# Performance work log

Measured on AMD Instinct MI355X. Metric: run time of the kernel, lower is better.

## Reference

```python
import jax, jax.numpy as jnp
import numpy as np

N, E, D_IN, D_HID, D_OUT = 50000, 800000, 128, 128, 300
BN_EPS = 1e-5


def setup_inputs() -> dict:
    key = jax.random.key(0)
    ks = jax.random.split(key, 10)
    s_in = 1.0 / np.sqrt(D_IN)
    s_hid = 1.0 / np.sqrt(D_HID)
    return {
        "x": jax.random.normal(ks[0], (N, D_IN), jnp.float32),
        "edge_index": jax.random.randint(ks[1], (2, E), 0, N, jnp.int64),
        "Wl": jax.random.normal(ks[2], (D_IN, D_HID), jnp.float32) * s_in,
        "bl": jnp.zeros((D_HID,), jnp.float32),
        "Wr": jax.random.normal(ks[3], (D_IN, D_HID), jnp.float32) * s_in,
        "Wsk": jax.random.normal(ks[4], (D_IN, D_HID), jnp.float32) * s_in,
        "bsk": jnp.zeros((D_HID,), jnp.float32),
        "gamma": jnp.ones((D_HID,), jnp.float32),
        "beta": jnp.zeros((D_HID,), jnp.float32),
        "rmean": jnp.zeros((D_HID,), jnp.float32),
        "rvar": jnp.ones((D_HID,), jnp.float32),
        "Wlo": jax.random.normal(ks[5], (D_HID, D_OUT), jnp.float32) * s_hid,
        "blo": jnp.zeros((D_OUT,), jnp.float32),
        "Wro": jax.random.normal(ks[6], (D_HID, D_OUT), jnp.float32) * s_hid,
    }


def sage_conv(x, src, dst, n_nodes, W_l, b_l, W_r):
    # PyG SAGEConv (aggr='mean'): lin_l(mean_{j in N(i)} x_j) + lin_r(x_i)
    msgs = x[src]                                                 # [E, d] gather
    agg = jax.ops.segment_sum(msgs, dst, num_segments=n_nodes)    # [N, d]
    cnt = jax.ops.segment_sum(jnp.ones((src.shape[0], 1), x.dtype), dst,
                              num_segments=n_nodes)               # [N, 1]
    mean = agg / jnp.maximum(cnt, 1.0)
    return mean @ W_l + b_l + x @ W_r


def reference(x, edge_index, Wl, bl, Wr, Wsk, bsk, gamma, beta, rmean, rvar,
              Wlo, blo, Wro):
    src, dst = edge_index[0], edge_index[1]
    n = x.shape[0]
    # layer 0: conv + skip linear
    h = sage_conv(x, src, dst, n, Wl, bl, Wr) + (x @ Wsk + bsk)
    # BatchNorm1d (eval: running stats)
    h = (h - rmean) * (gamma * jax.lax.rsqrt(rvar + BN_EPS)) + beta
    x_emb = jax.nn.relu(h)                                        # dropout: no-op in eval
    # output conv + log_softmax
    x_out = sage_conv(x_emb, src, dst, n, Wlo, blo, Wro)
    return h, jax.nn.log_softmax(x_out, axis=1)
```

## Files before the change

### kernel.cpp

```cpp
#include <hip/hip_runtime.h>

typedef __attribute__((__ext_vector_type__(8))) __bf16 bf16x8;
typedef __attribute__((__ext_vector_type__(4))) float f32x4;
typedef __attribute__((__ext_vector_type__(2))) float f32x2;
typedef __attribute__((__ext_vector_type__(4))) unsigned int u32x4;

__device__ __forceinline__ float bf2f(unsigned short u) {
    return __uint_as_float(((unsigned int)u) << 16);
}
__device__ __forceinline__ unsigned short f2bf(float f) {
    unsigned int u = __float_as_uint(f);
    u += 0x7FFFu + ((u >> 16) & 1u);
    return (unsigned short)(u >> 16);
}

__device__ __forceinline__ bool low_short_is_bf16like(unsigned int w) {
    unsigned int lo = w & 0xFFFFu;
    if (lo == 0u || lo == 0x8000u) return true;
    unsigned int e = (lo >> 7) & 0xFFu;
    return (e >= 0x6Cu && e <= 0x8Cu);
}
__device__ __forceinline__ int probe_f32(const unsigned int* __restrict__ p) {
    int t = threadIdx.x & 63;
    int cnt = __popcll(__ballot(low_short_is_bf16like(p[t])));
    return (cnt < 32) ? 1 : 0;
}
__device__ __forceinline__ int probe_e64(const unsigned int* __restrict__ ei) {
    int t = threadIdx.x & 63;
    unsigned int o1 = ei[2 * t + 1];
    unsigned int o2 = ei[2 * t + 129];
    return __all((o1 == 0u) && (o2 == 0u)) ? 1 : 0;
}

__global__ __launch_bounds__(256) void k_tobf(
    const void* __restrict__ xv, unsigned short* __restrict__ xbf,
    unsigned int* __restrict__ x8, int* __restrict__ deg,
    long nelem, int n, int tgrid)
{
    if ((int)blockIdx.x >= tgrid) {
        int j = ((int)blockIdx.x - tgrid) * 256 + threadIdx.x;
        if (j < n) deg[j] = 0;
        return;
    }
    int xf32 = probe_f32((const unsigned int*)xv);
    long i = ((long)blockIdx.x * 256 + threadIdx.x) * 8;
    if (i >= nelem) return;
    float f[8];
    if (xf32) {
        const float4* p = (const float4*)((const float*)xv + i);
        float4 v0 = p[0], v1 = p[1];
        f[0] = v0.x; f[1] = v0.y; f[2] = v0.z; f[3] = v0.w;
        f[4] = v1.x; f[5] = v1.y; f[6] = v1.z; f[7] = v1.w;
        u32x4 o;
        o.x = (unsigned int)f2bf(f[0]) | ((unsigned int)f2bf(f[1]) << 16);
        o.y = (unsigned int)f2bf(f[2]) | ((unsigned int)f2bf(f[3]) << 16);
        o.z = (unsigned int)f2bf(f[4]) | ((unsigned int)f2bf(f[5]) << 16);
        o.w = (unsigned int)f2bf(f[6]) | ((unsigned int)f2bf(f[7]) << 16);
        *(u32x4*)&xbf[i] = o;
    } else {
        u32x4 v = *(const u32x4*)((const unsigned short*)xv + i);
        *(u32x4*)&xbf[i] = v;
        f[0] = bf2f((unsigned short)v.x); f[1] = bf2f((unsigned short)(v.x >> 16));
        f[2] = bf2f((unsigned short)v.y); f[3] = bf2f((unsigned short)(v.y >> 16));
        f[4] = bf2f((unsigned short)v.z); f[5] = bf2f((unsigned short)(v.z >> 16));
        f[6] = bf2f((unsigned short)v.w); f[7] = bf2f((unsigned short)(v.w >> 16));
    }
    unsigned int q0 = 0, q1 = 0;
    q0 = (unsigned int)__builtin_amdgcn_cvt_pk_fp8_f32(f[0], f[1], (int)q0, false);
    q0 = (unsigned int)__builtin_amdgcn_cvt_pk_fp8_f32(f[2], f[3], (int)q0, true);
    q1 = (unsigned int)__builtin_amdgcn_cvt_pk_fp8_f32(f[4], f[5], (int)q1, false);
    q1 = (unsigned int)__builtin_amdgcn_cvt_pk_fp8_f32(f[6], f[7], (int)q1, true);
    uint2 q; q.x = q0; q.y = q1;
    *(uint2*)&x8[i >> 2] = q;
}

__global__ __launch_bounds__(256) void k_to8(
    const unsigned short* __restrict__ src, unsigned int* __restrict__ dst,
    long nelem)
{
    long i = ((long)blockIdx.x * 256 + threadIdx.x) * 8;
    if (i >= nelem) return;
    u32x4 v = *(const u32x4*)&src[i];
    unsigned int q0 = 0, q1 = 0;
    q0 = (unsigned int)__builtin_amdgcn_cvt_pk_fp8_f32(
            bf2f((unsigned short)v.x), bf2f((unsigned short)(v.x >> 16)), (int)q0, false);
    q0 = (unsigned int)__builtin_amdgcn_cvt_pk_fp8_f32(
            bf2f((unsigned short)v.y), bf2f((unsigned short)(v.y >> 16)), (int)q0, true);
    q1 = (unsigned int)__builtin_amdgcn_cvt_pk_fp8_f32(
            bf2f((unsigned short)v.z), bf2f((unsigned short)(v.z >> 16)), (int)q1, false);
    q1 = (unsigned int)__builtin_amdgcn_cvt_pk_fp8_f32(
            bf2f((unsigned short)v.w), bf2f((unsigned short)(v.w >> 16)), (int)q1, true);
    uint2 q; q.x = q0; q.y = q1;
    *(uint2*)&dst[i >> 2] = q;
}

__global__ __launch_bounds__(256) void k_fold(
    const void* __restrict__ Wl, const void* __restrict__ Wr,
    const void* __restrict__ Wsk, const void* __restrict__ gamma,
    const void* __restrict__ rvar, const void* __restrict__ bl,
    const void* __restrict__ bsk, const void* __restrict__ rmean,
    const void* __restrict__ beta, const void* __restrict__ Wlo,
    const void* __restrict__ blo, const void* __restrict__ Wro,
    unsigned short* __restrict__ W1p, unsigned short* __restrict__ W2p,
    float* __restrict__ bias1, float* __restrict__ bias2)
{
    int wf32 = probe_f32((const unsigned int*)Wl);
    int b = blockIdx.x, t = threadIdx.x;
    if (b < 128) {
        int idx = b * 256 + t;
        int kb = idx >> 10, c = (idx >> 3) & 127, k7 = idx & 7;
        int k = kb * 8 + k7;
        float g, rv, w;
        if (wf32) {
            g  = ((const float*)gamma)[c];
            rv = ((const float*)rvar)[c];
            if (k < 128) w = ((const float*)Wl)[k * 128 + c];
            else { int kk = k - 128;
                   w = ((const float*)Wr)[kk * 128 + c] + ((const float*)Wsk)[kk * 128 + c]; }
        } else {
            g  = bf2f(((const unsigned short*)gamma)[c]);
            rv = bf2f(((const unsigned short*)rvar)[c]);
            if (k < 128) w = bf2f(((const unsigned short*)Wl)[k * 128 + c]);
            else { int kk = k - 128;
                   w = bf2f(((const unsigned short*)Wr)[kk * 128 + c]) +
                       bf2f(((const unsigned short*)Wsk)[kk * 128 + c]); }
        }
        float s = g * rsqrtf(rv + 1e-5f);
        W1p[idx] = f2bf(w * s);
    } else if (b < 448) {
        int idx = (b - 128) * 256 + t;
        int kb = idx / 2560;
        int rem = idx - kb * 2560;
        int c = rem >> 3, k7 = idx & 7;
        int k = kb * 8 + k7;
        float w = 0.f;
        if (c < 300) {
            if (wf32)
                w = (k < 128) ? ((const float*)Wlo)[k * 300 + c]
                              : ((const float*)Wro)[(k - 128) * 300 + c];
            else
                w = (k < 128) ? bf2f(((const unsigned short*)Wlo)[k * 300 + c])
                              : bf2f(((const unsigned short*)Wro)[(k - 128) * 300 + c]);
        }
        W2p[idx] = f2bf(w);
    } else {
        if (t < 128) {
            float g, rv, b1, b2, rm, be;
            if (wf32) {
                g = ((const float*)gamma)[t]; rv = ((const float*)rvar)[t];
                b1 = ((const float*)bl)[t];   b2 = ((const float*)bsk)[t];
                rm = ((const float*)rmean)[t]; be = ((const float*)beta)[t];
            } else {
                g = bf2f(((const unsigned short*)gamma)[t]); rv = bf2f(((const unsigned short*)rvar)[t]);
                b1 = bf2f(((const unsigned short*)bl)[t]);   b2 = bf2f(((const unsigned short*)bsk)[t]);
                rm = bf2f(((const unsigned short*)rmean)[t]); be = bf2f(((const unsigned short*)beta)[t]);
            }
            float s = g * rsqrtf(rv + 1e-5f);
            bias1[t] = (b1 + b2 - rm) * s + be;
        }
        for (int c = t; c < 320; c += 256) {
            float v = 0.f;
            if (c < 300)
                v = wf32 ? ((const float*)blo)[c] : bf2f(((const unsigned short*)blo)[c]);
            bias2[c] = v;
        }
    }
}

__global__ __launch_bounds__(256) void k_rank(
    const int* __restrict__ ei,
    int* __restrict__ deg, int* __restrict__ rank, int E, int nnodes)
{
    int e64 = probe_e64((const unsigned int*)ei);
    int e = blockIdx.x * 256 + threadIdx.x;
    if (e >= E) return;
    int d = e64 ? ei[2 * (E + e)] : ei[E + e];
    int r = 0;
    if ((unsigned)d < (unsigned)nnodes) r = atomicAdd(&deg[d], 1);
    rank[e] = r;
}

template <typename IT>
__global__ __launch_bounds__(256) void k_place(
    const int* __restrict__ ei,
    const int* __restrict__ rowptr, const int* __restrict__ aux,
    const int* __restrict__ rank,
    IT* __restrict__ adj, int E, int nnodes)
{
    int e64 = probe_e64((const unsigned int*)ei);
    int e = blockIdx.x * 256 + threadIdx.x;
    if (e >= E) return;
    int s, d;
    if (e64) { s = ei[2 * e]; d = ei[2 * (E + e)]; }
    else     { s = ei[e];     d = ei[E + e]; }
    if ((unsigned)d >= (unsigned)nnodes) return;
    if ((unsigned)s >= (unsigned)nnodes) s = 0;
    adj[rowptr[d] + aux[d >> 10] + rank[e]] = (IT)s;
}

__global__ __launch_bounds__(256) void k_scan_a(
    const int* __restrict__ deg, int* __restrict__ rowptr,
    int* __restrict__ aux, int n)
{
    __shared__ int wsum[4];
    int t = threadIdx.x, blk = blockIdx.x;
    int base = blk * 1024 + t * 4;
    int v[4];
    int s = 0;
    #pragma unroll
    for (int i = 0; i < 4; i++) { int idx = base + i; v[i] = (idx < n) ? deg[idx] : 0; s += v[i]; }
    int lane = t & 63, wv = t >> 6;
    int inc = s;
    #pragma unroll
    for (int off = 1; off < 64; off <<= 1) {
        int u = __shfl_up(inc, off);
        if (lane >= off) inc += u;
    }
    if (lane == 63) wsum[wv] = inc;
    __syncthreads();
    int woff = 0;
    if (wv >= 1) woff += wsum[0];
    if (wv >= 2) woff += wsum[1];
    if (wv >= 3) woff += wsum[2];
    int exc = woff + inc - s;
    #pragma unroll
    for (int i = 0; i < 4; i++) { int idx = base + i; if (idx < n) rowptr[idx] = exc; exc += v[i]; }
    if (t == 255) aux[blk] = woff + inc;
}

__global__ __launch_bounds__(64) void k_scan_b(int* __restrict__ aux, int nblk)
{
    int t = threadIdx.x;
    int carry = 0;
    for (int base = 0; base < nblk; base += 64) {
        int idx = base + t;
        int v = (idx < nblk) ? aux[idx] : 0;
        int inc = v;
        #pragma unroll
        for (int off = 1; off < 64; off <<= 1) {
            int u = __shfl_up(inc, off);
            if (t >= off) inc += u;
        }
        if (idx < nblk) aux[idx] = carry + inc - v;
        carry += __shfl(inc, 63);
    }
}

template <typename IT>
__global__ __launch_bounds__(256) void k_agg(
    const unsigned int* __restrict__ x8,
    const int* __restrict__ rowptr, const int* __restrict__ aux,
    const int* __restrict__ deg,
    const IT* __restrict__ adj, unsigned short* __restrict__ meanB, int n)
{
    int wid = (blockIdx.x * 256 + threadIdx.x) >> 6;
    if (wid >= n) return;
    int lane = threadIdx.x & 63;
    int h  = lane >> 5;
    int sl = lane & 31;
    int start = rowptr[wid] + aux[wid >> 10];
    int dc = deg[wid];
    float acc[4][4];
    #pragma unroll
    for (int u = 0; u < 4; u++)
        #pragma unroll
        for (int c = 0; c < 4; c++) acc[u][c] = 0.f;
    int i = 0;
    for (; i + 7 < dc; i += 8) {
        int e0 = (int)adj[start + i + h];
        int e1 = (int)adj[start + i + 2 + h];
        int e2 = (int)adj[start + i + 4 + h];
        int e3 = (int)adj[start + i + 6 + h];
        unsigned int p0 = x8[(size_t)e0 * 32 + sl];
        unsigned int p1 = x8[(size_t)e1 * 32 + sl];
        unsigned int p2 = x8[(size_t)e2 * 32 + sl];
        unsigned int p3 = x8[(size_t)e3 * 32 + sl];
        f32x2 l0 = __builtin_amdgcn_cvt_pk_f32_fp8((int)p0, false);
        f32x2 h0 = __builtin_amdgcn_cvt_pk_f32_fp8((int)p0, true);
        f32x2 l1 = __builtin_amdgcn_cvt_pk_f32_fp8((int)p1, false);
        f32x2 h1 = __builtin_amdgcn_cvt_pk_f32_fp8((int)p1, true);
        f32x2 l2 = __builtin_amdgcn_cvt_pk_f32_fp8((int)p2, false);
        f32x2 h2 = __builtin_amdgcn_cvt_pk_f32_fp8((int)p2, true);
        f32x2 l3 = __builtin_amdgcn_cvt_pk_f32_fp8((int)p3, false);
        f32x2 h3 = __builtin_amdgcn_cvt_pk_f32_fp8((int)p3, true);
        acc[0][0] += l0.x; acc[0][1] += l0.y; acc[0][2] += h0.x; acc[0][3] += h0.y;
        acc[1][0] += l1.x; acc[1][1] += l1.y; acc[1][2] += h1.x; acc[1][3] += h1.y;
        acc[2][0] += l2.x; acc[2][1] += l2.y; acc[2][2] += h2.x; acc[2][3] += h2.y;
        acc[3][0] += l3.x; acc[3][1] += l3.y; acc[3][2] += h3.x; acc[3][3] += h3.y;
    }
    for (; i + h < dc; i += 2) {
        int e0 = (int)adj[start + i + h];
        unsigned int p0 = x8[(size_t)e0 * 32 + sl];
        f32x2 l0 = __builtin_amdgcn_cvt_pk_f32_fp8((int)p0, false);
        f32x2 h0 = __builtin_amdgcn_cvt_pk_f32_fp8((int)p0, true);
        acc[0][0] += l0.x; acc[0][1] += l0.y; acc[0][2] += h0.x; acc[0][3] += h0.y;
    }
    float t0 = (acc[0][0] + acc[1][0]) + (acc[2][0] + acc[3][0]);
    float t1 = (acc[0][1] + acc[1][1]) + (acc[2][1] + acc[3][1]);
    float t2 = (acc[0][2] + acc[1][2]) + (acc[2][2] + acc[3][2]);
    float t3 = (acc[0][3] + acc[1][3]) + (acc[2][3] + acc[3][3]);
    t0 += __shfl_xor(t0, 32);
    t1 += __shfl_xor(t1, 32);
    t2 += __shfl_xor(t2, 32);
    t3 += __shfl_xor(t3, 32);
    if (h == 0) {
        float inv = 1.f / fmaxf((float)dc, 1.f);
        uint2 o;
        o.x = (unsigned int)f2bf(t0 * inv) | ((unsigned int)f2bf(t1 * inv) << 16);
        o.y = (unsigned int)f2bf(t2 * inv) | ((unsigned int)f2bf(t3 * inv) << 16);
        *(uint2*)&meanB[(size_t)wid * 128 + sl * 4] = o;
    }
}

__global__ __launch_bounds__(256) void k_gemm1(
    const unsigned short* __restrict__ meanB,
    const unsigned short* __restrict__ xbf, const unsigned int* __restrict__ xprobe,
    const unsigned short* __restrict__ Wp,
    const float* __restrict__ bias, void* __restrict__ outh,
    unsigned short* __restrict__ xemb, int nrows)
{
    constexpr int NTW = 2;
    __shared__ __align__(16) unsigned short Alds[32 * 264];
    int tid = threadIdx.x;
    int row0 = blockIdx.x * 32;
    int xf32 = probe_f32(xprobe);
    {
        int r = tid >> 3, c0 = (tid & 7) * 16;
        int rg = row0 + r; if (rg >= nrows) rg = nrows - 1;
        const u32x4* mp = (const u32x4*)(meanB + (size_t)rg * 128 + c0);
        *(u32x4*)&Alds[r * 264 + c0]     = mp[0];
        *(u32x4*)&Alds[r * 264 + c0 + 8] = mp[1];
        const u32x4* xp = (const u32x4*)(xbf + (size_t)rg * 128 + c0);
        *(u32x4*)&Alds[r * 264 + 128 + c0]     = xp[0];
        *(u32x4*)&Alds[r * 264 + 128 + c0 + 8] = xp[1];
    }
    __syncthreads();
    f32x4 acc[2][NTW];
    #pragma unroll
    for (int a = 0; a < 2; a++)
        #pragma unroll
        for (int b = 0; b < NTW; b++) acc[a][b] = f32x4{0.f, 0.f, 0.f, 0.f};
    int lane = tid & 63, wv = tid >> 6, lh = lane & 15, lq = lane >> 4;
    #pragma unroll
    for (int ks = 0; ks < 8; ++ks) {
        bf16x8 a0 = *(const bf16x8*)&Alds[lh * 264 + ks * 32 + lq * 8];
        bf16x8 a1 = *(const bf16x8*)&Alds[(16 + lh) * 264 + ks * 32 + lq * 8];
        #pragma unroll
        for (int i = 0; i < NTW; i++) {
            int col = (wv + 4 * i) * 16 + lh;
            bf16x8 bfr = *(const bf16x8*)&Wp[(ks * 4 + lq) * 1024 + col * 8];
            acc[0][i] = __builtin_amdgcn_mfma_f32_16x16x32_bf16(a0, bfr, acc[0][i], 0, 0, 0);
            acc[1][i] = __builtin_amdgcn_mfma_f32_16x16x32_bf16(a1, bfr, acc[1][i], 0, 0, 0);
        }
    }
    float* outF = (float*)outh;
    unsigned short* outB = (unsigned short*)outh;
    #pragma unroll
    for (int rt = 0; rt < 2; ++rt)
        #pragma unroll
        for (int i = 0; i < NTW; i++)
            #pragma unroll
            for (int j = 0; j < 4; j++) {
                int r = row0 + rt * 16 + lq * 4 + j;
                if (r < nrows) {
                    int c = (wv + 4 * i) * 16 + lh;
                    float v = acc[rt][i][j] + bias[c];
                    if (xf32) outF[(size_t)r * 128 + c] = v;
                    else      outB[(size_t)r * 128 + c] = f2bf(v);
                    xemb[(size_t)r * 128 + c] = f2bf(fmaxf(v, 0.f));
                }
            }
}

__global__ __launch_bounds__(256) void k_gemm2(
    const unsigned short* __restrict__ meanB,
    const unsigned short* __restrict__ xf, const unsigned int* __restrict__ xprobe,
    const unsigned short* __restrict__ Wp,
    const float* __restrict__ bias, void* __restrict__ outbase, int nrows)
{
    constexpr int NTW = 5;
    __shared__ __align__(16) unsigned short Alds[32 * 264];
    __shared__ float redM[4][32];
    __shared__ float redS[4][32];
    int tid = threadIdx.x;
    int row0 = blockIdx.x * 32;
    int xf32 = probe_f32(xprobe);
    {
        int r = tid >> 3, c0 = (tid & 7) * 16;
        int rg = row0 + r; if (rg >= nrows) rg = nrows - 1;
        const u32x4* mp = (const u32x4*)(meanB + (size_t)rg * 128 + c0);
        *(u32x4*)&Alds[r * 264 + c0]     = mp[0];
        *(u32x4*)&Alds[r * 264 + c0 + 8] = mp[1];
        const u32x4* xp = (const u32x4*)(xf + (size_t)rg * 128 + c0);
        *(u32x4*)&Alds[r * 264 + 128 + c0]     = xp[0];
        *(u32x4*)&Alds[r * 264 + 128 + c0 + 8] = xp[1];
    }
    __syncthreads();
    f32x4 acc[2][NTW];
    #pragma unroll
    for (int a = 0; a < 2; a++)
        #pragma unroll
        for (int b = 0; b < NTW; b++) acc[a][b] = f32x4{0.f, 0.f, 0.f, 0.f};
    int lane = tid & 63, wv = tid >> 6, lh = lane & 15, lq = lane >> 4;
    #pragma unroll
    for (int ks = 0; ks < 8; ++ks) {
        bf16x8 a0 = *(const bf16x8*)&Alds[lh * 264 + ks * 32 + lq * 8];
        bf16x8 a1 = *(const bf16x8*)&Alds[(16 + lh) * 264 + ks * 32 + lq * 8];
        #pragma unroll
        for (int i = 0; i < NTW; i++) {
            int col = (wv + 4 * i) * 16 + lh;
            bf16x8 bfr = *(const bf16x8*)&Wp[(ks * 4 + lq) * 2560 + col * 8];
            acc[0][i] = __builtin_amdgcn_mfma_f32_16x16x32_bf16(a0, bfr, acc[0][i], 0, 0, 0);
            acc[1][i] = __builtin_amdgcn_mfma_f32_16x16x32_bf16(a1, bfr, acc[1][i], 0, 0, 0);
        }
    }
    #pragma unroll
    for (int rt = 0; rt < 2; ++rt)
        #pragma unroll
        for (int i = 0; i < NTW; i++) {
            int col = (wv + 4 * i) * 16 + lh;
            float b = bias[col];
            #pragma unroll
            for (int j = 0; j < 4; j++) acc[rt][i][j] += b;
        }
    float M[2][4];
    #pragma unroll
    for (int rt = 0; rt < 2; ++rt)
        #pragma unroll
        for (int j = 0; j < 4; j++) {
            float m = -3.0e38f;
            #pragma unroll
            for (int i = 0; i < NTW; i++) {
                int col = (wv + 4 * i) * 16 + lh;
                if (col < 300) m = fmaxf(m, acc[rt][i][j]);
            }
            m = fmaxf(m, __shfl_xor(m, 1, 16));
            m = fmaxf(m, __shfl_xor(m, 2, 16));
            m = fmaxf(m, __shfl_xor(m, 4, 16));
            m = fmaxf(m, __shfl_xor(m, 8, 16));
            M[rt][j] = m;
        }
    if (lh == 0) {
        #pragma unroll
        for (int rt = 0; rt < 2; ++rt)
            #pragma unroll
            for (int j = 0; j < 4; j++)
                redM[wv][rt * 16 + lq * 4 + j] = M[rt][j];
    }
    __syncthreads();
    #pragma unroll
    for (int rt = 0; rt < 2; ++rt)
        #pragma unroll
        for (int j = 0; j < 4; j++) {
            int rl = rt * 16 + lq * 4 + j;
            M[rt][j] = fmaxf(fmaxf(redM[0][rl], redM[1][rl]),
                             fmaxf(redM[2][rl], redM[3][rl]));
        }
    float S[2][4];
    #pragma unroll
    for (int rt = 0; rt < 2; ++rt)
        #pragma unroll
        for (int j = 0; j < 4; j++) {
            float s = 0.f;
            #pragma unroll
            for (int i = 0; i < NTW; i++) {
                int col = (wv + 4 * i) * 16 + lh;
                if (col < 300) s += __expf(acc[rt][i][j] - M[rt][j]);
            }
            s += __shfl_xor(s, 1, 16);
            s += __shfl_xor(s, 2, 16);
            s += __shfl_xor(s, 4, 16);
            s += __shfl_xor(s, 8, 16);
            S[rt][j] = s;
        }
    if (lh == 0) {
        #pragma unroll
        for (int rt = 0; rt < 2; ++rt)
            #pragma unroll
            for (int j = 0; j < 4; j++)
                redS[wv][rt * 16 + lq * 4 + j] = S[rt][j];
    }
    __syncthreads();
    float* out1F = (float*)outbase + (size_t)nrows * 128;
    unsigned short* out1B = (unsigned short*)outbase + (size_t)nrows * 128;
    #pragma unroll
    for (int rt = 0; rt < 2; ++rt)
        #pragma unroll
        for (int j = 0; j < 4; j++) {
            int rl = rt * 16 + lq * 4 + j;
            float Sall = (redS[0][rl] + redS[1][rl]) + (redS[2][rl] + redS[3][rl]);
            float L = M[rt][j] + __logf(Sall);
            int rg = row0 + rl;
            if (rg < nrows) {
                #pragma unroll
                for (int i = 0; i < NTW; i++) {
                    int col = (wv + 4 * i) * 16 + lh;
                    if (col < 300) {
                        float v = acc[rt][i][j] - L;
                        if (xf32) out1F[(size_t)rg * 300 + col] = v;
                        else      out1B[(size_t)rg * 300 + col] = f2bf(v);
                    }
                }
            }
        }
}

extern "C" void kernel_launch(void* const* d_in, const int* in_sizes, int n_in,
                              void* d_out, int out_size, void* d_ws, size_t ws_size,
                              hipStream_t stream)
{
    const void* x     = d_in[0];
    const int*  ei    = (const int*)d_in[1];
    const void* Wl    = d_in[2];
    const void* bl    = d_in[3];
    const void* Wr    = d_in[4];
    const void* Wsk   = d_in[5];
    const void* bsk   = d_in[6];
    const void* gamma = d_in[7];
    const void* beta  = d_in[8];
    const void* rmean = d_in[9];
    const void* rvar  = d_in[10];
    const void* Wlo   = d_in[11];
    const void* blo   = d_in[12];
    const void* Wro   = d_in[13];

    int N = in_sizes[0] / 128;
    int E = in_sizes[1] / 2;
    long nelem = (long)N * 128;
    bool idx16 = (N <= 65535);

    char* ws = (char*)d_ws;
    size_t off = 0;
    unsigned short* xbf   = (unsigned short*)(ws + off); off += (size_t)N * 128 * 2;
    unsigned short* meanB = (unsigned short*)(ws + off); off += (size_t)N * 128 * 2;
    unsigned short* xemb  = (unsigned short*)(ws + off); off += (size_t)N * 128 * 2;
    unsigned int* x8      = (unsigned int*)(ws + off);   off += (size_t)N * 128;
    unsigned int* xemb8   = (unsigned int*)(ws + off);   off += (size_t)N * 128;
    off = (off + 255) & ~(size_t)255;
    int* deg    = (int*)(ws + off);           off += (size_t)N * 4;
    int* rowptr = (int*)(ws + off);           off += (size_t)N * 4;
    int* rank   = (int*)(ws + off);           off += (size_t)E * 4;
    int* aux    = (int*)(ws + off);           off += 256;
    void* adjv  = (void*)(ws + off);          off += (size_t)E * 4;
    off = (off + 255) & ~(size_t)255;
    unsigned short* W1p = (unsigned short*)(ws + off);  off += 32768 * 2;
    unsigned short* W2p = (unsigned short*)(ws + off);  off += 81920 * 2;
    float* bias1 = (float*)(ws + off);        off += 512;
    float* bias2 = (float*)(ws + off);        off += 1280;

    int egrid = (E + 255) / 256;
    int sblk  = (N + 1023) / 1024;
    int agrid = (N + 3) / 4;
    int ggrid = (N + 31) / 32;
    int tgrid = (int)((nelem / 8 + 255) / 256);
    int dgrid = (N + 255) / 256;

    const unsigned int* xprobe = (const unsigned int*)x;

    k_tobf<<<tgrid + dgrid, 256, 0, stream>>>(x, xbf, x8, deg, nelem, N, tgrid);
    k_fold<<<449, 256, 0, stream>>>(Wl, Wr, Wsk, gamma, rvar, bl, bsk, rmean, beta,
                                    Wlo, blo, Wro, W1p, W2p, bias1, bias2);

    k_rank<<<egrid, 256, 0, stream>>>(ei, deg, rank, E, N);
    k_scan_a<<<sblk, 256, 0, stream>>>(deg, rowptr, aux, N);
    k_scan_b<<<1, 64, 0, stream>>>(aux, sblk);

    if (idx16) {
        unsigned short* adj = (unsigned short*)adjv;
        k_place<unsigned short><<<egrid, 256, 0, stream>>>(ei, rowptr, aux, rank, adj, E, N);
        k_agg<unsigned short><<<agrid, 256, 0, stream>>>(x8, rowptr, aux, deg, adj, meanB, N);
        k_gemm1<<<ggrid, 256, 0, stream>>>(meanB, xbf, xprobe, W1p, bias1, d_out, xemb, N);
        k_to8<<<tgrid, 256, 0, stream>>>(xemb, xemb8, nelem);
        k_agg<unsigned short><<<agrid, 256, 0, stream>>>(xemb8, rowptr, aux, deg, adj, meanB, N);
        k_gemm2<<<ggrid, 256, 0, stream>>>(meanB, xemb, xprobe, W2p, bias2, d_out, N);
    } else {
        int* adj = (int*)adjv;
        k_place<int><<<egrid, 256, 0, stream>>>(ei, rowptr, aux, rank, adj, E, N);
        k_agg<int><<<agrid, 256, 0, stream>>>(x8, rowptr, aux, deg, adj, meanB, N);
        k_gemm1<<<ggrid, 256, 0, stream>>>(meanB, xbf, xprobe, W1p, bias1, d_out, xemb, N);
        k_to8<<<tgrid, 256, 0, stream>>>(xemb, xemb8, nelem);
        k_agg<int><<<agrid, 256, 0, stream>>>(xemb8, rowptr, aux, deg, adj, meanB, N);
        k_gemm2<<<ggrid, 256, 0, stream>>>(meanB, xemb, xprobe, W2p, bias2, d_out, N);
    }
}
```

Before: 176.7 us.

## Fuse fp8 quantization of embeddings into gemm1 epilogue and deepen gather unroll

Removes the separate k_to8 kernel. The gemm1 epilogue now stages the ReLU'd bf16 embedding tile in LDS and writes the fp8 copy directly, which saves a launch and a full re-read of xemb. The aggregation loop is unrolled to 16 neighbors per iteration with 8 outstanding gathers per lane, giving more memory-level parallelism at the cost of registers. Float outputs use nontemporal stores to reduce cache pollution. The extra LDS round trip and barriers add some epilogue cost.

Result: no change. 179.6 us (+1.6%).

```diff
diff --git a/kernel.cpp b/kernel.cpp
--- a/kernel.cpp
+++ b/kernel.cpp
@@ -74,26 +74,6 @@
     *(uint2*)&x8[i >> 2] = q;
 }
 
-__global__ __launch_bounds__(256) void k_to8(
-    const unsigned short* __restrict__ src, unsigned int* __restrict__ dst,
-    long nelem)
-{
-    long i = ((long)blockIdx.x * 256 + threadIdx.x) * 8;
-    if (i >= nelem) return;
-    u32x4 v = *(const u32x4*)&src[i];
-    unsigned int q0 = 0, q1 = 0;
-    q0 = (unsigned int)__builtin_amdgcn_cvt_pk_fp8_f32(
-            bf2f((unsigned short)v.x), bf2f((unsigned short)(v.x >> 16)), (int)q0, false);
-    q0 = (unsigned int)__builtin_amdgcn_cvt_pk_fp8_f32(
-            bf2f((unsigned short)v.y), bf2f((unsigned short)(v.y >> 16)), (int)q0, true);
-    q1 = (unsigned int)__builtin_amdgcn_cvt_pk_fp8_f32(
-            bf2f((unsigned short)v.z), bf2f((unsigned short)(v.z >> 16)), (int)q1, false);
-    q1 = (unsigned int)__builtin_amdgcn_cvt_pk_fp8_f32(
-            bf2f((unsigned short)v.w), bf2f((unsigned short)(v.w >> 16)), (int)q1, true);
-    uint2 q; q.x = q0; q.y = q1;
-    *(uint2*)&dst[i >> 2] = q;
-}
-
 __global__ __launch_bounds__(256) void k_fold(
     const void* __restrict__ Wl, const void* __restrict__ Wr,
     const void* __restrict__ Wsk, const void* __restrict__ gamma,
@@ -266,34 +246,41 @@
         #pragma unroll
         for (int c = 0; c < 4; c++) acc[u][c] = 0.f;
     int i = 0;
-    for (; i + 7 < dc; i += 8) {
-        int e0 = (int)adj[start + i + h];
-        int e1 = (int)adj[start + i + 2 + h];
-        int e2 = (int)adj[start + i + 4 + h];
-        int e3 = (int)adj[start + i + 6 + h];
-        unsigned int p0 = x8[(size_t)e0 * 32 + sl];
-        unsigned int p1 = x8[(size_t)e1 * 32 + sl];
-        unsigned int p2 = x8[(size_t)e2 * 32 + sl];
-        unsigned int p3 = x8[(size_t)e3 * 32 + sl];
-        f32x2 l0 = __builtin_amdgcn_cvt_pk_f32_fp8((int)p0, false);
-        f32x2 h0 = __builtin_amdgcn_cvt_pk_f32_fp8((int)p0, true);
-        f32x2 l1 = __builtin_amdgcn_cvt_pk_f32_fp8((int)p1, false);
-        f32x2 h1 = __builtin_amdgcn_cvt_pk_f32_fp8((int)p1, true);
-        f32x2 l2 = __builtin_amdgcn_cvt_pk_f32_fp8((int)p2, false);
-        f32x2 h2 = __builtin_amdgcn_cvt_pk_f32_fp8((int)p2, true);
-        f32x2 l3 = __builtin_amdgcn_cvt_pk_f32_fp8((int)p3, false);
-        f32x2 h3 = __builtin_amdgcn_cvt_pk_f32_fp8((int)p3, true);
-        acc[0][0] += l0.x; acc[0][1] += l0.y; acc[0][2] += h0.x; acc[0][3] += h0.y;
-        acc[1][0] += l1.x; acc[1][1] += l1.y; acc[1][2] += h1.x; acc[1][3] += h1.y;
-        acc[2][0] += l2.x; acc[2][1] += l2.y; acc[2][2] += h2.x; acc[2][3] += h2.y;
-        acc[3][0] += l3.x; acc[3][1] += l3.y; acc[3][2] += h3.x; acc[3][3] += h3.y;
+    for (; i + 15 < dc; i += 16) {
+        int e[8]; unsigned int p[8];
+        #pragma unroll
+        for (int u = 0; u < 8; u++) e[u] = (int)adj[start + i + 2 * u + h];
+        #pragma unroll
+        for (int u = 0; u < 8; u++) p[u] = x8[(size_t)e[u] * 32 + sl];
+        #pragma unroll
+        for (int u = 0; u < 8; u++) {
+            f32x2 lo = __builtin_amdgcn_cvt_pk_f32_fp8((int)p[u], false);
+            f32x2 hi = __builtin_amdgcn_cvt_pk_f32_fp8((int)p[u], true);
+            acc[u & 3][0] += lo.x; acc[u & 3][1] += lo.y;
+            acc[u & 3][2] += hi.x; acc[u & 3][3] += hi.y;
+        }
+    }
+    if (i + 7 < dc) {
+        int e[4]; unsigned int p[4];
+        #pragma unroll
+        for (int u = 0; u < 4; u++) e[u] = (int)adj[start + i + 2 * u + h];
+        #pragma unroll
+        for (int u = 0; u < 4; u++) p[u] = x8[(size_t)e[u] * 32 + sl];
+        #pragma unroll
+        for (int u = 0; u < 4; u++) {
+            f32x2 lo = __builtin_amdgcn_cvt_pk_f32_fp8((int)p[u], false);
+            f32x2 hi = __builtin_amdgcn_cvt_pk_f32_fp8((int)p[u], true);
+            acc[u][0] += lo.x; acc[u][1] += lo.y;
+            acc[u][2] += hi.x; acc[u][3] += hi.y;
+        }
+        i += 8;
     }
     for (; i + h < dc; i += 2) {
         int e0 = (int)adj[start + i + h];
         unsigned int p0 = x8[(size_t)e0 * 32 + sl];
-        f32x2 l0 = __builtin_amdgcn_cvt_pk_f32_fp8((int)p0, false);
-        f32x2 h0 = __builtin_amdgcn_cvt_pk_f32_fp8((int)p0, true);
-        acc[0][0] += l0.x; acc[0][1] += l0.y; acc[0][2] += h0.x; acc[0][3] += h0.y;
+        f32x2 lo = __builtin_amdgcn_cvt_pk_f32_fp8((int)p0, false);
+        f32x2 hi = __builtin_amdgcn_cvt_pk_f32_fp8((int)p0, true);
+        acc[0][0] += lo.x; acc[0][1] += lo.y; acc[0][2] += hi.x; acc[0][3] += hi.y;
     }
     float t0 = (acc[0][0] + acc[1][0]) + (acc[2][0] + acc[3][0]);
     float t1 = (acc[0][1] + acc[1][1]) + (acc[2][1] + acc[3][1]);
@@ -317,7 +304,7 @@
     const unsigned short* __restrict__ xbf, const unsigned int* __restrict__ xprobe,
     const unsigned short* __restrict__ Wp,
     const float* __restrict__ bias, void* __restrict__ outh,
-    unsigned short* __restrict__ xemb, int nrows)
+    unsigned short* __restrict__ xemb, unsigned int* __restrict__ xemb8, int nrows)
 {
     constexpr int NTW = 2;
     __shared__ __align__(16) unsigned short Alds[32 * 264];
@@ -353,6 +340,7 @@
             acc[1][i] = __builtin_amdgcn_mfma_f32_16x16x32_bf16(a1, bfr, acc[1][i], 0, 0, 0);
         }
     }
+    __syncthreads();
     float* outF = (float*)outh;
     unsigned short* outB = (unsigned short*)outh;
     #pragma unroll
@@ -361,15 +349,55 @@
         for (int i = 0; i < NTW; i++)
             #pragma unroll
             for (int j = 0; j < 4; j++) {
-                int r = row0 + rt * 16 + lq * 4 + j;
+                int rl = rt * 16 + lq * 4 + j;
+                int r = row0 + rl;
+                int c = (wv + 4 * i) * 16 + lh;
+                float v = acc[rt][i][j] + bias[c];
+                float rv = fmaxf(v, 0.f);
+                unsigned short rb = f2bf(rv);
+                Alds[rl * 264 + c] = rb;
                 if (r < nrows) {
-                    int c = (wv + 4 * i) * 16 + lh;
-                    float v = acc[rt][i][j] + bias[c];
-                    if (xf32) outF[(size_t)r * 128 + c] = v;
+                    if (xf32) __builtin_nontemporal_store(v, &outF[(size_t)r * 128 + c]);
                     else      outB[(size_t)r * 128 + c] = f2bf(v);
-                    xemb[(size_t)r * 128 + c] = f2bf(fmaxf(v, 0.f));
+                    xemb[(size_t)r * 128 + c] = rb;
                 }
             }
+    __syncthreads();
+    {
+        int r = tid >> 3, c0 = (tid & 7) * 16;
+        int rg = row0 + r;
+        if (rg < nrows) {
+            u32x4 va = *(u32x4*)&Alds[r * 264 + c0];
+            u32x4 vb = *(u32x4*)&Alds[r * 264 + c0 + 8];
+            u32x4 q;
+            unsigned int w;
+            w = 0;
+            w = (unsigned int)__builtin_amdgcn_cvt_pk_fp8_f32(
+                    bf2f((unsigned short)va.x), bf2f((unsigned short)(va.x >> 16)), (int)w, false);
+            w = (unsigned int)__builtin_amdgcn_cvt_pk_fp8_f32(
+                    bf2f((unsigned short)va.y), bf2f((unsigned short)(va.y >> 16)), (int)w, true);
+            q.x = w;
+            w = 0;
+            w = (unsigned int)__builtin_amdgcn_cvt_pk_fp8_f32(
+                    bf2f((unsigned short)va.z), bf2f((unsigned short)(va.z >> 16)), (int)w, false);
+            w = (unsigned int)__builtin_amdgcn_cvt_pk_fp8_f32(
+                    bf2f((unsigned short)va.w), bf2f((unsigned short)(va.w >> 16)), (int)w, true);
+            q.y = w;
+            w = 0;
+            w = (unsigned int)__builtin_amdgcn_cvt_pk_fp8_f32(
+                    bf2f((unsigned short)vb.x), bf2f((unsigned short)(vb.x >> 16)), (int)w, false);
+            w = (unsigned int)__builtin_amdgcn_cvt_pk_fp8_f32(
+                    bf2f((unsigned short)vb.y), bf2f((unsigned short)(vb.y >> 16)), (int)w, true);
+            q.z = w;
+            w = 0;
+            w = (unsigned int)__builtin_amdgcn_cvt_pk_fp8_f32(
+                    bf2f((unsigned short)vb.z), bf2f((unsigned short)(vb.z >> 16)), (int)w, false);
+            w = (unsigned int)__builtin_amdgcn_cvt_pk_fp8_f32(
+                    bf2f((unsigned short)vb.w), bf2f((unsigned short)(vb.w >> 16)), (int)w, true);
+            q.w = w;
+            *(u32x4*)&xemb8[(size_t)rg * 32 + (tid & 7) * 4] = q;
+        }
+    }
 }
 
 __global__ __launch_bounds__(256) void k_gemm2(
@@ -497,7 +525,7 @@
                     int col = (wv + 4 * i) * 16 + lh;
                     if (col < 300) {
                         float v = acc[rt][i][j] - L;
-                        if (xf32) out1F[(size_t)rg * 300 + col] = v;
+                        if (xf32) __builtin_nontemporal_store(v, &out1F[(size_t)rg * 300 + col]);
                         else      out1B[(size_t)rg * 300 + col] = f2bf(v);
                     }
                 }
@@ -569,16 +597,14 @@
         unsigned short* adj = (unsigned short*)adjv;
         k_place<unsigned short><<<egrid, 256, 0, stream>>>(ei, rowptr, aux, rank, adj, E, N);
         k_agg<unsigned short><<<agrid, 256, 0, stream>>>(x8, rowptr, aux, deg, adj, meanB, N);
-        k_gemm1<<<ggrid, 256, 0, stream>>>(meanB, xbf, xprobe, W1p, bias1, d_out, xemb, N);
-        k_to8<<<tgrid, 256, 0, stream>>>(xemb, xemb8, nelem);
+        k_gemm1<<<ggrid, 256, 0, stream>>>(meanB, xbf, xprobe, W1p, bias1, d_out, xemb, xemb8, N);
         k_agg<unsigned short><<<agrid, 256, 0, stream>>>(xemb8, rowptr, aux, deg, adj, meanB, N);
         k_gemm2<<<ggrid, 256, 0, stream>>>(meanB, xemb, xprobe, W2p, bias2, d_out, N);
     } else {
         int* adj = (int*)adjv;
         k_place<int><<<egrid, 256, 0, stream>>>(ei, rowptr, aux, rank, adj, E, N);
         k_agg<int><<<agrid, 256, 0, stream>>>(x8, rowptr, aux, deg, adj, meanB, N);
-        k_gemm1<<<ggrid, 256, 0, stream>>>(meanB, xbf, xprobe, W1p, bias1, d_out, xemb, N);
-        k_to8<<<tgrid, 256, 0, stream>>>(xemb, xemb8, nelem);
+        k_gemm1<<<ggrid, 256, 0, stream>>>(meanB, xbf, xprobe, W1p, bias1, d_out, xemb, xemb8, N);
         k_agg<int><<<agrid, 256, 0, stream>>>(xemb8, rowptr, aux, deg, adj, meanB, N);
         k_gemm2<<<ggrid, 256, 0, stream>>>(meanB, xemb, xprobe, W2p, bias2, d_out, N);
     }
```
